# Performance work log

Hardware: AMD Instinct MI355X
Metric: run time of the kernel (lower is better)

## Reference

```python
import jax, jax.numpy as jnp
import numpy as np

T_DF = 10.0  # t-distribution degrees of freedom used in _t_dist_sim


def setup_inputs() -> dict:
    key = jax.random.key(0)
    ks = jax.random.split(key, 16)
    B, D, H, Z, K = 4096, 10000, 128, 32, 16
    s = lambda k, sh, fan: jax.random.normal(k, sh, jnp.float32) * (1.0 / np.sqrt(fan))
    return {
        "x": jax.random.normal(ks[0], (B, D), jnp.float32),
        "enc_w1": s(ks[1], (D, H), D), "enc_b1": jnp.zeros((H,), jnp.float32),
        "enc_w2": s(ks[2], (H, Z), H), "enc_b2": jnp.zeros((Z,), jnp.float32),
        "embeddings": jax.random.normal(ks[3], (K, Z), jnp.float32) * 0.05,
        "dec_e_w1": s(ks[4], (Z, H), Z), "dec_e_b1": jnp.zeros((H,), jnp.float32),
        "dec_e_w2": s(ks[5], (H, D), H), "dec_e_b2": jnp.zeros((D,), jnp.float32),
        "dec_q_w1": s(ks[6], (Z, H), Z), "dec_q_b1": jnp.zeros((H,), jnp.float32),
        "dec_q_w2": s(ks[7], (H, D), H), "dec_q_b2": jnp.zeros((D,), jnp.float32),
    }


def _mlp(h, w1, b1, w2, b2):
    # Linear -> ReLU -> Linear (dropout inactive at inference)
    return jax.nn.relu(h @ w1 + b1) @ w2 + b2


def reference(x, enc_w1, enc_b1, enc_w2, enc_b2, embeddings,
              dec_e_w1, dec_e_b1, dec_e_w2, dec_e_b2,
              dec_q_w1, dec_q_b1, dec_q_w2, dec_q_b2):
    # Encoder: x [B,D] -> z_e [B,Z]
    z_e = _mlp(x, enc_w1, enc_b1, enc_w2, enc_b2)
    # Squared euclidean distance to centroids: [B,K]
    z_dist = jnp.sum((z_e[:, None, :] - embeddings[None, :, :]) ** 2, axis=-1)
    # t-distribution kernel + row normalization
    dist_prob = (1.0 + z_dist / T_DF) ** (-(T_DF + 1.0) / 2.0)
    dist_prob = dist_prob / jnp.sum(dist_prob, axis=1, keepdims=True)
    k = jnp.argmax(dist_prob, axis=-1)            # [B] cluster assignments
    z_q = embeddings[k]                           # vectorized gather [B,Z]
    x_q = _mlp(z_q, dec_q_w1, dec_q_b1, dec_q_w2, dec_q_b2)
    x_e = _mlp(z_e, dec_e_w1, dec_e_b1, dec_e_w2, dec_e_b2)
    return (x_e, x_q, z_e, z_q, k, z_dist, dist_prob)
```

## Files before the change

kernel.cpp:

```cpp
#include <hip/hip_runtime.h>

#define B_N 4096
#define D_N 10000
#define H_N 128
#define Z_N 32
#define K_N 16

#define OUT_XE 0ull
#define OUT_XQ 40960000ull
#define OUT_ZE 81920000ull
#define OUT_ZQ 82051072ull
#define OUT_K  82182144ull
#define OUT_ZD 82186240ull
#define OUT_DP 82251776ull

#define WS_PART 0ull
#define WS_H1   16777216ull
#define WS_HE   18874368ull
#define WS_HQ   19922944ull
#define WS_W2TE 20971520ull
#define WS_W2TQ 23543808ull

typedef short bf16x8 __attribute__((ext_vector_type(8)));
typedef float f32x4  __attribute__((ext_vector_type(4)));

static __device__ __forceinline__ unsigned short f2bf(float f) {
    union { float f; unsigned u; } v; v.f = f;
    return (unsigned short)((v.u + 0x7fffu + ((v.u >> 16) & 1u)) >> 16);
}

__global__ __launch_bounds__(256) void transpose_cvt_kernel(
        const float* __restrict__ we, const float* __restrict__ wq,
        unsigned* __restrict__ oe, unsigned* __restrict__ oq) {
    const float* w2 = blockIdx.y ? wq : we;
    unsigned* o = blockIdx.y ? oq : oe;
    __shared__ float lds[64 * 129];
    const int n0 = blockIdx.x * 64;
    const int t = threadIdx.x;
#pragma unroll
    for (int i = 0; i < 32; ++i) {
        int idx = t + 256 * i;
        int k = idx >> 6, n = idx & 63;
        float v = (n0 + n < D_N) ? w2[(size_t)k * D_N + n0 + n] : 0.f;
        lds[n * 129 + k] = v;
    }
    __syncthreads();
#pragma unroll
    for (int i = 0; i < 16; ++i) {
        int idx = t + 256 * i;
        int n = idx >> 6, c = idx & 63;
        unsigned lo = f2bf(lds[n * 129 + 2 * c]);
        unsigned hi = f2bf(lds[n * 129 + 2 * c + 1]);
        o[(size_t)(n0 + n) * 64 + c] = lo | (hi << 16);
    }
}

__global__ __launch_bounds__(256) void gemm1_kernel(
        const float* __restrict__ x, const float* __restrict__ w1, float* __restrict__ part) {
    __shared__ float xs[32 * 64];
    __shared__ float wsm[32 * 128];
    const int t = threadIdx.x;
    const int m0 = blockIdx.x * 64;
    const int dstart = blockIdx.y * 1252;
    const int rg = (t >> 5) * 8;
    const int cg = (t & 31) * 4;
    float acc[8][4];
#pragma unroll
    for (int i = 0; i < 8; ++i)
#pragma unroll
        for (int j = 0; j < 4; ++j) acc[i][j] = 0.f;

    for (int dc = 0; dc < 40; ++dc) {
        __syncthreads();
#pragma unroll
        for (int i = 0; i < 2; ++i) {
            int idx = t + 256 * i;
            int r = idx & 63, cv = idx >> 6;
            int dl = dc * 32 + cv * 4;
            bool ok = (dl < 1252) && (dstart + dl < D_N);
            float4 v = ok ? *(const float4*)&x[(size_t)(m0 + r) * D_N + dstart + dl]
                          : make_float4(0.f, 0.f, 0.f, 0.f);
            int ddb = cv * 4;
            xs[(ddb + 0) * 64 + r] = v.x;
            xs[(ddb + 1) * 64 + r] = v.y;
            xs[(ddb + 2) * 64 + r] = v.z;
            xs[(ddb + 3) * 64 + r] = v.w;
        }
#pragma unroll
        for (int i = 0; i < 4; ++i) {
            int idx = t + 256 * i;
            int dd = idx >> 5, hv = (idx & 31) * 4;
            int dl = dc * 32 + dd;
            bool ok = (dl < 1252) && (dstart + dl < D_N);
            float4 v = ok ? *(const float4*)&w1[(size_t)(dstart + dl) * H_N + hv]
                          : make_float4(0.f, 0.f, 0.f, 0.f);
            *(float4*)&wsm[dd * H_N + hv] = v;
        }
        __syncthreads();
#pragma unroll 4
        for (int dd = 0; dd < 32; ++dd) {
            float4 wv = *(float4*)&wsm[dd * H_N + cg];
            float4 xa = *(float4*)&xs[dd * 64 + rg];
            float4 xb = *(float4*)&xs[dd * 64 + rg + 4];
            float xr[8] = {xa.x, xa.y, xa.z, xa.w, xb.x, xb.y, xb.z, xb.w};
            float wr[4] = {wv.x, wv.y, wv.z, wv.w};
#pragma unroll
            for (int i = 0; i < 8; ++i)
#pragma unroll
                for (int j = 0; j < 4; ++j) acc[i][j] += xr[i] * wr[j];
        }
    }
    float* pb = part + (size_t)blockIdx.y * (B_N * H_N);
#pragma unroll
    for (int i = 0; i < 8; ++i) {
        *(float4*)&pb[(size_t)(m0 + rg + i) * H_N + cg] =
            make_float4(acc[i][0], acc[i][1], acc[i][2], acc[i][3]);
    }
}

__global__ __launch_bounds__(256) void reduce_kernel(
        const float* __restrict__ part, const float* __restrict__ b1, float* __restrict__ h1) {
    int idx = blockIdx.x * 256 + threadIdx.x;
    int h = idx & 127;
    float s = b1[h];
#pragma unroll
    for (int ks = 0; ks < 8; ++ks) s += part[(size_t)ks * (B_N * H_N) + idx];
    h1[idx] = fmaxf(s, 0.f);
}

__global__ __launch_bounds__(256) void cluster_kernel(
        const float* __restrict__ h1, const float* __restrict__ w2,
        const float* __restrict__ b2, const float* __restrict__ emb,
        float* __restrict__ out) {
    const int t = threadIdx.x;
    const int l = t & 63;
    const int m = blockIdx.x * 4 + (t >> 6);
    const int c = l & 31, half = l >> 5;
    const float* hrow = h1 + (size_t)m * H_N;
    float acc = 0.f;
#pragma unroll 8
    for (int j = 0; j < 64; ++j) {
        int hh = half * 64 + j;
        acc += hrow[hh] * w2[hh * Z_N + c];
    }
    acc += __shfl_xor(acc, 32);
    float z = acc + b2[c];
    if (l < 32) out[OUT_ZE + (size_t)m * Z_N + l] = z;

    const int k = l & 15, quad = l >> 4;
    float dk = 0.f;
#pragma unroll
    for (int j = 0; j < 8; ++j) {
        int cc = quad * 8 + j;
        float zc = __shfl(z, cc);
        float d = zc - emb[k * Z_N + cc];
        dk += d * d;
    }
    dk += __shfl_xor(dk, 16);
    dk += __shfl_xor(dk, 32);

    float p = powf(1.0f + dk * 0.1f, -5.5f);
    float s = p;
    s += __shfl_xor(s, 1); s += __shfl_xor(s, 2);
    s += __shfl_xor(s, 4); s += __shfl_xor(s, 8);
    float prob = p / s;

    int bi = 0;
    float best = __shfl(p, 0);
#pragma unroll
    for (int kk = 1; kk < 16; ++kk) {
        float pk = __shfl(p, kk);
        if (pk > best) { best = pk; bi = kk; }
    }
    if (l < 16) {
        out[OUT_ZD + (size_t)m * K_N + l] = dk;
        out[OUT_DP + (size_t)m * K_N + l] = prob;
    }
    if (l == 0) out[OUT_K + m] = (float)bi;
    if (l < 32) out[OUT_ZQ + (size_t)m * Z_N + l] = emb[bi * Z_N + l];
}

__global__ __launch_bounds__(256) void dec1_kernel(
        const float* __restrict__ out,
        const float* __restrict__ w1e, const float* __restrict__ b1e,
        const float* __restrict__ w1q, const float* __restrict__ b1q,
        unsigned short* __restrict__ he, unsigned short* __restrict__ hq) {
    int idx = blockIdx.x * 256 + threadIdx.x;
    int m = idx >> 7, h = idx & 127;
    const float* w1; const float* b1; const float* zrow; unsigned short* o;
    if (blockIdx.y == 0) { w1 = w1e; b1 = b1e; zrow = out + OUT_ZE; o = he; }
    else                 { w1 = w1q; b1 = b1q; zrow = out + OUT_ZQ; o = hq; }
    zrow += (size_t)m * Z_N;
    float acc = b1[h];
#pragma unroll 8
    for (int z = 0; z < Z_N; ++z) acc += zrow[z] * w1[z * H_N + h];
    o[idx] = f2bf(fmaxf(acc, 0.f));
}

__global__ __launch_bounds__(256) void dec2_kernel(
        const unsigned short* __restrict__ he, const unsigned short* __restrict__ hq,
        const unsigned short* __restrict__ w2te, const unsigned short* __restrict__ w2tq,
        const float* __restrict__ b2e, const float* __restrict__ b2q,
        float* __restrict__ out) {
    const unsigned short* hptr; const unsigned short* wt; const float* b2; float* o;
    if (blockIdx.z == 0) { hptr = he; wt = w2te; b2 = b2e; o = out + OUT_XE; }
    else                 { hptr = hq; wt = w2tq; b2 = b2q; o = out + OUT_XQ; }
    const int t = threadIdx.x;
    const int l = t & 63, w = t >> 6;
    const int m0 = blockIdx.x * 64;
    const int n0 = blockIdx.y * 256 + w * 64;
    if (n0 >= D_N) return;
    const int lane16 = l & 15, quad = l >> 4;

    f32x4 acc[4][4];
#pragma unroll
    for (int i = 0; i < 4; ++i)
#pragma unroll
        for (int j = 0; j < 4; ++j) acc[i][j] = (f32x4){0.f, 0.f, 0.f, 0.f};

#pragma unroll
    for (int ks = 0; ks < 4; ++ks) {
        const int koff = ks * 32 + quad * 8;
        bf16x8 a[4], bb[4];
#pragma unroll
        for (int mi = 0; mi < 4; ++mi)
            a[mi] = *(const bf16x8*)&hptr[(size_t)(m0 + mi * 16 + lane16) * H_N + koff];
#pragma unroll
        for (int ni = 0; ni < 4; ++ni)
            bb[ni] = *(const bf16x8*)&wt[(size_t)(n0 + ni * 16 + lane16) * H_N + koff];
#pragma unroll
        for (int mi = 0; mi < 4; ++mi)
#pragma unroll
            for (int ni = 0; ni < 4; ++ni)
                acc[mi][ni] = __builtin_amdgcn_mfma_f32_16x16x32_bf16(
                    a[mi], bb[ni], acc[mi][ni], 0, 0, 0);
    }
#pragma unroll
    for (int ni = 0; ni < 4; ++ni) {
        int gn = n0 + ni * 16 + lane16;
        if (gn >= D_N) continue;
        float bias = b2[gn];
#pragma unroll
        for (int mi = 0; mi < 4; ++mi) {
            int gmb = m0 + mi * 16 + quad * 4;
#pragma unroll
            for (int r = 0; r < 4; ++r)
                o[(size_t)(gmb + r) * D_N + gn] = acc[mi][ni][r] + bias;
        }
    }
}

extern "C" void kernel_launch(void* const* d_in, const int* in_sizes, int n_in,
                              void* d_out, int out_size, void* d_ws, size_t ws_size,
                              hipStream_t stream) {
    const float* x      = (const float*)d_in[0];
    const float* enc_w1 = (const float*)d_in[1];
    const float* enc_b1 = (const float*)d_in[2];
    const float* enc_w2 = (const float*)d_in[3];
    const float* enc_b2 = (const float*)d_in[4];
    const float* emb    = (const float*)d_in[5];
    const float* de_w1  = (const float*)d_in[6];
    const float* de_b1  = (const float*)d_in[7];
    const float* de_w2  = (const float*)d_in[8];
    const float* de_b2  = (const float*)d_in[9];
    const float* dq_w1  = (const float*)d_in[10];
    const float* dq_b1  = (const float*)d_in[11];
    const float* dq_w2  = (const float*)d_in[12];
    const float* dq_b2  = (const float*)d_in[13];

    float* out = (float*)d_out;
    char* ws = (char*)d_ws;
    float* part           = (float*)(ws + WS_PART);
    float* h1             = (float*)(ws + WS_H1);
    unsigned short* he    = (unsigned short*)(ws + WS_HE);
    unsigned short* hq    = (unsigned short*)(ws + WS_HQ);
    unsigned short* w2te  = (unsigned short*)(ws + WS_W2TE);
    unsigned short* w2tq  = (unsigned short*)(ws + WS_W2TQ);

    transpose_cvt_kernel<<<dim3(157, 2), 256, 0, stream>>>(de_w2, dq_w2,
                                                           (unsigned*)w2te, (unsigned*)w2tq);
    gemm1_kernel<<<dim3(64, 8), 256, 0, stream>>>(x, enc_w1, part);
    reduce_kernel<<<2048, 256, 0, stream>>>(part, enc_b1, h1);
    cluster_kernel<<<1024, 256, 0, stream>>>(h1, enc_w2, enc_b2, emb, out);
    dec1_kernel<<<dim3(2048, 2), 256, 0, stream>>>(out, de_w1, de_b1, dq_w1, dq_b1, he, hq);
    dec2_kernel<<<dim3(64, 40, 2), 256, 0, stream>>>(he, hq, w2te, w2tq, de_b2, dq_b2, out);
}
```

Measured before the change: 780.8 us.

## Run encoder GEMM on fp16 MFMA with split-precision hi/lo operands

Replaces the scalar FP32 LDS-tiled encoder GEMM with MFMA 16x16x32 fp16 instructions. Each operand is scaled and split into fp16 high and low parts, and three MFMAs per tile recover near-FP32 accuracy. A new pre-pass kernel transposes and splits enc_w1 into a padded K-major layout, using the not-yet-written x_e output region as scratch. The scale factors are undone in the reduce kernel. The aim is to remove the FMA-bound inner loop, at the cost of an extra weight prep pass, fp16 overflow and underflow risk from the scaling, and direct uncoalesced global B loads without LDS staging.

Result: faster. 736.8 us (-5.6%).

```diff
diff --git a/kernel.cpp b/kernel.cpp
--- a/kernel.cpp
+++ b/kernel.cpp
@@ -5,6 +5,8 @@
 #define H_N 128
 #define Z_N 32
 #define K_N 16
+#define KPAD 10240
+#define KSLICE 1280
 
 #define OUT_XE 0ull
 #define OUT_XQ 40960000ull
@@ -22,6 +24,7 @@
 #define WS_W2TQ 23543808ull
 
 typedef short bf16x8 __attribute__((ext_vector_type(8)));
+typedef _Float16 half8 __attribute__((ext_vector_type(8)));
 typedef float f32x4  __attribute__((ext_vector_type(4)));
 
 static __device__ __forceinline__ unsigned short f2bf(float f) {
@@ -55,77 +58,106 @@
     }
 }
 
+__global__ __launch_bounds__(256) void w1t_kernel(
+        const float* __restrict__ w1, unsigned* __restrict__ th, unsigned* __restrict__ tl) {
+    __shared__ float lds[128 * 66];
+    const int t = threadIdx.x;
+    const int d0 = blockIdx.x * 64;
+#pragma unroll
+    for (int i = 0; i < 32; ++i) {
+        int idx = t + 256 * i;
+        int dl = idx >> 7, h = idx & 127;
+        float v = (d0 + dl < D_N) ? w1[(size_t)(d0 + dl) * H_N + h] : 0.f;
+        lds[h * 66 + dl] = v;
+    }
+    __syncthreads();
+#pragma unroll
+    for (int i = 0; i < 16; ++i) {
+        int idx = t + 256 * i;
+        int h = idx >> 5, c = idx & 31;
+        float f0 = lds[h * 66 + 2 * c]     * 2048.f;
+        float f1 = lds[h * 66 + 2 * c + 1] * 2048.f;
+        _Float16 h0 = (_Float16)f0, h1 = (_Float16)f1;
+        _Float16 l0 = (_Float16)(f0 - (float)h0);
+        _Float16 l1 = (_Float16)(f1 - (float)h1);
+        union { _Float16 hh[2]; unsigned u; } ph, pl;
+        ph.hh[0] = h0; ph.hh[1] = h1;
+        pl.hh[0] = l0; pl.hh[1] = l1;
+        size_t o = (size_t)h * (KPAD / 2) + blockIdx.x * 32 + c;
+        th[o] = ph.u;
+        tl[o] = pl.u;
+    }
+}
+
 __global__ __launch_bounds__(256) void gemm1_kernel(
-        const float* __restrict__ x, const float* __restrict__ w1, float* __restrict__ part) {
-    __shared__ float xs[32 * 64];
-    __shared__ float wsm[32 * 128];
-    const int t = threadIdx.x;
-    const int m0 = blockIdx.x * 64;
-    const int dstart = blockIdx.y * 1252;
-    const int rg = (t >> 5) * 8;
-    const int cg = (t & 31) * 4;
-    float acc[8][4];
-#pragma unroll
-    for (int i = 0; i < 8; ++i)
-#pragma unroll
-        for (int j = 0; j < 4; ++j) acc[i][j] = 0.f;
-
-    for (int dc = 0; dc < 40; ++dc) {
-        __syncthreads();
-#pragma unroll
-        for (int i = 0; i < 2; ++i) {
-            int idx = t + 256 * i;
-            int r = idx & 63, cv = idx >> 6;
-            int dl = dc * 32 + cv * 4;
-            bool ok = (dl < 1252) && (dstart + dl < D_N);
-            float4 v = ok ? *(const float4*)&x[(size_t)(m0 + r) * D_N + dstart + dl]
-                          : make_float4(0.f, 0.f, 0.f, 0.f);
-            int ddb = cv * 4;
-            xs[(ddb + 0) * 64 + r] = v.x;
-            xs[(ddb + 1) * 64 + r] = v.y;
-            xs[(ddb + 2) * 64 + r] = v.z;
-            xs[(ddb + 3) * 64 + r] = v.w;
+        const float* __restrict__ x,
+        const unsigned short* __restrict__ w1th,
+        const unsigned short* __restrict__ w1tl,
+        float* __restrict__ part) {
+    const int t = threadIdx.x;
+    const int l = t & 63, w = t >> 6;
+    const int lane16 = l & 15, quad = l >> 4;
+    const int m = blockIdx.x * 64 + w * 16 + lane16;
+    const int dstart = blockIdx.y * KSLICE;
+
+    f32x4 acc[8];
+#pragma unroll
+    for (int i = 0; i < 8; ++i) acc[i] = (f32x4){0.f, 0.f, 0.f, 0.f};
+
+    const float* xrow = x + (size_t)m * D_N;
+    const unsigned short* bhb = w1th + (size_t)lane16 * KPAD + quad * 8;
+    const unsigned short* blb = w1tl + (size_t)lane16 * KPAD + quad * 8;
+
+    for (int step = 0; step < 40; ++step) {
+        const int kg = dstart + step * 32;
+        if (kg >= D_N) break;
+        const int kl = kg + quad * 8;
+        float xv[8];
+        if (kg + 32 <= D_N) {
+            float4 v0 = *(const float4*)&xrow[kl];
+            float4 v1 = *(const float4*)&xrow[kl + 4];
+            xv[0] = v0.x; xv[1] = v0.y; xv[2] = v0.z; xv[3] = v0.w;
+            xv[4] = v1.x; xv[5] = v1.y; xv[6] = v1.z; xv[7] = v1.w;
+        } else {
+#pragma unroll
+            for (int j = 0; j < 8; ++j)
+                xv[j] = (kl + j < D_N) ? xrow[kl + j] : 0.f;
         }
-#pragma unroll
-        for (int i = 0; i < 4; ++i) {
-            int idx = t + 256 * i;
-            int dd = idx >> 5, hv = (idx & 31) * 4;
-            int dl = dc * 32 + dd;
-            bool ok = (dl < 1252) && (dstart + dl < D_N);
-            float4 v = ok ? *(const float4*)&w1[(size_t)(dstart + dl) * H_N + hv]
-                          : make_float4(0.f, 0.f, 0.f, 0.f);
-            *(float4*)&wsm[dd * H_N + hv] = v;
+        half8 ah, al;
+#pragma unroll
+        for (int j = 0; j < 8; ++j) {
+            float f = xv[j] * 2048.f;
+            _Float16 hv = (_Float16)f;
+            ah[j] = hv;
+            al[j] = (_Float16)(f - (float)hv);
         }
-        __syncthreads();
-#pragma unroll 4
-        for (int dd = 0; dd < 32; ++dd) {
-            float4 wv = *(float4*)&wsm[dd * H_N + cg];
-            float4 xa = *(float4*)&xs[dd * 64 + rg];
-            float4 xb = *(float4*)&xs[dd * 64 + rg + 4];
-            float xr[8] = {xa.x, xa.y, xa.z, xa.w, xb.x, xb.y, xb.z, xb.w};
-            float wr[4] = {wv.x, wv.y, wv.z, wv.w};
-#pragma unroll
-            for (int i = 0; i < 8; ++i)
-#pragma unroll
-                for (int j = 0; j < 4; ++j) acc[i][j] += xr[i] * wr[j];
+#pragma unroll
+        for (int ni = 0; ni < 8; ++ni) {
+            const size_t off = (size_t)ni * (16 * KPAD) + kg;
+            half8 bh = *(const half8*)(bhb + off);
+            half8 bl = *(const half8*)(blb + off);
+            acc[ni] = __builtin_amdgcn_mfma_f32_16x16x32_f16(ah, bh, acc[ni], 0, 0, 0);
+            acc[ni] = __builtin_amdgcn_mfma_f32_16x16x32_f16(al, bh, acc[ni], 0, 0, 0);
+            acc[ni] = __builtin_amdgcn_mfma_f32_16x16x32_f16(ah, bl, acc[ni], 0, 0, 0);
         }
     }
-    float* pb = part + (size_t)blockIdx.y * (B_N * H_N);
-#pragma unroll
-    for (int i = 0; i < 8; ++i) {
-        *(float4*)&pb[(size_t)(m0 + rg + i) * H_N + cg] =
-            make_float4(acc[i][0], acc[i][1], acc[i][2], acc[i][3]);
-    }
+    float* pb = part + (size_t)blockIdx.y * (B_N * H_N)
+              + (size_t)(blockIdx.x * 64 + w * 16 + quad * 4) * H_N;
+#pragma unroll
+    for (int ni = 0; ni < 8; ++ni)
+#pragma unroll
+        for (int r = 0; r < 4; ++r)
+            pb[(size_t)r * H_N + ni * 16 + lane16] = acc[ni][r];
 }
 
 __global__ __launch_bounds__(256) void reduce_kernel(
         const float* __restrict__ part, const float* __restrict__ b1, float* __restrict__ h1) {
     int idx = blockIdx.x * 256 + threadIdx.x;
     int h = idx & 127;
-    float s = b1[h];
+    float s = 0.f;
 #pragma unroll
     for (int ks = 0; ks < 8; ++ks) s += part[(size_t)ks * (B_N * H_N) + idx];
-    h1[idx] = fmaxf(s, 0.f);
+    h1[idx] = fmaxf(s * (1.0f / 4194304.0f) + b1[h], 0.f);
 }
 
 __global__ __launch_bounds__(256) void cluster_kernel(
@@ -276,10 +308,13 @@
     unsigned short* hq    = (unsigned short*)(ws + WS_HQ);
     unsigned short* w2te  = (unsigned short*)(ws + WS_W2TE);
     unsigned short* w2tq  = (unsigned short*)(ws + WS_W2TQ);
-
+    unsigned short* w1th  = (unsigned short*)out;
+    unsigned short* w1tl  = (unsigned short*)out + (size_t)H_N * KPAD;
+
+    w1t_kernel<<<dim3(KPAD / 64), 256, 0, stream>>>(enc_w1, (unsigned*)w1th, (unsigned*)w1tl);
     transpose_cvt_kernel<<<dim3(157, 2), 256, 0, stream>>>(de_w2, dq_w2,
                                                            (unsigned*)w2te, (unsigned*)w2tq);
-    gemm1_kernel<<<dim3(64, 8), 256, 0, stream>>>(x, enc_w1, part);
+    gemm1_kernel<<<dim3(64, 8), 256, 0, stream>>>(x, w1th, w1tl, part);
     reduce_kernel<<<2048, 256, 0, stream>>>(part, enc_b1, h1);
     cluster_kernel<<<1024, 256, 0, stream>>>(h1, enc_w2, enc_b2, emb, out);
     dec1_kernel<<<dim3(2048, 2), 256, 0, stream>>>(out, de_w1, de_b1, dq_w1, dq_b1, he, hq);
```
